# Kernel tuning notes

Measured on AMD Instinct MI355X. Metric: run time of the kernel, lower is better.

Reference implementation:

```python
import jax, jax.numpy as jnp
import numpy as np

G = 256       # number of graphs in batch
NPG = 400     # nodes per graph (hardcoded in module)
DEG = 32      # avg degree
FIN = 400     # input feature dim
H = 64        # hidden_channels
N = G * NPG
E = G * NPG * DEG


def _glorot(key, fan_in, fan_out):
    lim = float(np.sqrt(6.0 / (fan_in + fan_out)))
    return jax.random.uniform(key, (fan_in, fan_out), jnp.float32, -lim, lim)


def setup_inputs() -> dict:
    key = jax.random.key(0)
    ks = jax.random.split(key, 12)
    x = jax.random.normal(ks[0], (N, FIN), jnp.float32)
    # intra-graph random edges, then offset by graph id so edges never cross graphs
    src = jax.random.randint(ks[1], (G, NPG * DEG), 0, NPG)
    dst = jax.random.randint(ks[2], (G, NPG * DEG), 0, NPG)
    offs = (jnp.arange(G) * NPG)[:, None]
    edge_index = jnp.stack([(src + offs).reshape(-1), (dst + offs).reshape(-1)]).astype(jnp.int32)
    edge_weight = jax.random.uniform(ks[3], (E,), jnp.float32)
    return {
        "x": x,
        "edge_index": edge_index,
        "edge_weight": edge_weight,
        "W1": _glorot(ks[4], FIN, H), "b1": jnp.zeros((H,), jnp.float32),
        "W2": _glorot(ks[5], H, H),   "b2": jnp.zeros((H,), jnp.float32),
        "W3": _glorot(ks[6], H, H),   "b3": jnp.zeros((H,), jnp.float32),
        "Wc": _glorot(ks[7], NPG * H, H), "bc": jnp.zeros((H,), jnp.float32),
        "Wl": _glorot(ks[8], H, 2),   "bl": jnp.zeros((2,), jnp.float32),
    }


def _gcn_conv(x, W, b, row, col, norm, n):
    # PyG GCNConv: out[col] += norm * (x @ W)[row]; then + bias
    h = x @ W                                   # [n, out]
    msg = norm[:, None] * h[row]                # [E+n, out] gather + scale
    return jax.ops.segment_sum(msg, col, num_segments=n) + b


def reference(x, edge_index, edge_weight, W1, b1, W2, b2, W3, b3, Wc, bc, Wl, bl):
    n = x.shape[0]
    loop = jnp.arange(n, dtype=edge_index.dtype)
    row = jnp.concatenate([edge_index[0], loop])            # sources (with self-loops)
    col = jnp.concatenate([edge_index[1], loop])            # targets
    ew = jnp.concatenate([edge_weight, jnp.ones((n,), edge_weight.dtype)])
    # symmetric normalization: deg^{-1/2}[row] * w * deg^{-1/2}[col]
    deg = jax.ops.segment_sum(ew, col, num_segments=n)
    dinv = jnp.where(deg > 0, jax.lax.rsqrt(deg), 0.0)
    norm = dinv[row] * ew * dinv[col]

    h = jax.nn.relu(_gcn_conv(x, W1, b1, row, col, norm, n))
    h = jax.nn.relu(_gcn_conv(h, W2, b2, row, col, norm, n))
    h = _gcn_conv(h, W3, b3, row, col, norm, n)
    # per-graph flatten of 400 nodes -> lincomb (vectorized form of the Python loop)
    g = h.reshape(-1, NPG * H) @ Wc + bc        # [G, H]
    # dropout p=0.5 skipped (eval mode)
    return g @ Wl + bl                          # [G, 2]
```

## Files before the change

kernel.cpp:

```cpp
#include <hip/hip_runtime.h>
#include <hip/hip_bf16.h>
#include <stdint.h>

#define G 256
#define NPG 400
#define DEG 32
#define FIN 400
#define H 64
#define NN (G*NPG)
#define EE (G*NPG*DEG)
#define EPG (NPG*DEG)
#define CPG (EPG+NPG)
#define NTILE 25
#define ATS 420
#define HTS 72
#define MTSZ 25600

#define W1F_OFF 0
#define W1F_N   (13*4*64*8)
#define W2F_OFF (W1F_OFF + W1F_N)
#define W2F_N   (2*4*64*8)
#define W3F_OFF (W2F_OFF + W2F_N)
#define WCF_OFF (W3F_OFF + W2F_N)
#define WCF_N   (800*4*64*8)
#define WF_TOT  (WCF_OFF + WCF_N)

typedef __attribute__((ext_vector_type(8))) _Float16 h8;
typedef __attribute__((ext_vector_type(4))) float f32x4;

static __device__ __forceinline__ unsigned packh2(float a, float b) {
  unsigned short ua = __builtin_bit_cast(unsigned short, (_Float16)a);
  unsigned short ub = __builtin_bit_cast(unsigned short, (_Float16)b);
  return (unsigned)ua | ((unsigned)ub << 16);
}

static __device__ __forceinline__ h8 cvt8(float4 a, float4 b) {
  h8 r;
  r[0] = (_Float16)a.x; r[1] = (_Float16)a.y; r[2] = (_Float16)a.z; r[3] = (_Float16)a.w;
  r[4] = (_Float16)b.x; r[5] = (_Float16)b.y; r[6] = (_Float16)b.z; r[7] = (_Float16)b.w;
  return r;
}

__global__ __launch_bounds__(256) void kPack(
    const float* __restrict__ W1, const float* __restrict__ W2,
    const float* __restrict__ W3, const float* __restrict__ Wc,
    _Float16* __restrict__ wf, float* __restrict__ gbuf)
{
  int idx = blockIdx.x*256 + threadIdx.x;
  if (idx < G*H) gbuf[idx] = 0.f;
  if (idx >= WF_TOT) return;
  if (idx < W2F_OFF) {
    int i = idx;
    int j = i & 7, ln = (i >> 3) & 63, nt = (i >> 9) & 3, ks = i >> 11;
    int k = ks*32 + (ln >> 4)*8 + j, col = nt*16 + (ln & 15);
    wf[idx] = (k < FIN) ? (_Float16)W1[k*H + col] : (_Float16)0.f;
  } else if (idx < W3F_OFF) {
    int i = idx - W2F_OFF;
    int j = i & 7, ln = (i >> 3) & 63, nt = (i >> 9) & 3, ks = i >> 11;
    wf[idx] = (_Float16)W2[(ks*32 + (ln >> 4)*8 + j)*H + nt*16 + (ln & 15)];
  } else if (idx < WCF_OFF) {
    int i = idx - W3F_OFF;
    int j = i & 7, ln = (i >> 3) & 63, nt = (i >> 9) & 3, ks = i >> 11;
    wf[idx] = (_Float16)W3[(ks*32 + (ln >> 4)*8 + j)*H + nt*16 + (ln & 15)];
  } else {
    int i = idx - WCF_OFF;
    int j = i & 7, ln = (i >> 3) & 63, nt = (i >> 9) & 3, kt = i >> 11;
    int kp = kt*32 + (ln >> 4)*8 + j;
    int node = kp % 400, feat = kp / 400;
    int col = nt*16 + (ln & 15);
    wf[idx] = (_Float16)Wc[((size_t)node*64 + feat)*64 + col];
  }
}

__global__ __launch_bounds__(1024) void kNorm(
    const int* __restrict__ ei, const float* __restrict__ ew,
    uint2* __restrict__ ent, uint32_t* __restrict__ boff)
{
  __shared__ float deg[NPG];
  __shared__ float dv[NPG];
  __shared__ uint32_t bcnt[32], bpos[32];
  const int g = blockIdx.x, tid = threadIdx.x;
  const int ebase = g*EPG, nbase = g*NPG;
  const int* rowp = ei;
  const int* colp = ei + EE;
  if (tid < NTILE) bcnt[tid] = 0u;
  for (int v = tid; v < NPG; v += 1024) deg[v] = 1.0f;
  __syncthreads();
  for (int e = tid; e < EPG; e += 1024) {
    int c = colp[ebase+e] - nbase;
    atomicAdd(&deg[c], ew[ebase+e]);
    atomicAdd(&bcnt[c >> 4], 1u);
  }
  __syncthreads();
  for (int v = tid; v < NPG; v += 1024) dv[v] = rsqrtf(deg[v]);
  if (tid == 0) {
    uint32_t s = 0;
    #pragma unroll
    for (int t = 0; t < NTILE; ++t) {
      uint32_t c = bcnt[t] + 16u;
      bcnt[t] = s; bpos[t] = s; s += c;
    }
  }
  __syncthreads();
  if (tid < NTILE) boff[g*32 + tid] = bcnt[tid];
  if (tid == NTILE) boff[g*32 + NTILE] = (uint32_t)CPG;
  uint2* eb = ent + (size_t)g*CPG;
  for (int e = tid; e < EPG; e += 1024) {
    int src = rowp[ebase+e] - nbase;
    int dst = colp[ebase+e] - nbase;
    float nm = dv[src] * ew[ebase+e] * dv[dst];
    uint32_t p = atomicAdd(&bpos[dst >> 4], 1u);
    eb[p] = make_uint2(((unsigned)dst << 16) | (unsigned)src, __float_as_uint(nm));
  }
  for (int v = tid; v < NPG; v += 1024) {
    uint32_t p = atomicAdd(&bpos[v >> 4], 1u);
    eb[p] = make_uint2(((unsigned)v << 16) | (unsigned)v, __float_as_uint(dv[v]*dv[v]));
  }
}

__global__ __launch_bounds__(256, 4) void kM1(
    const float* __restrict__ x, const _Float16* __restrict__ wf,
    _Float16* __restrict__ mt1)
{
  __shared__ _Float16 sh[64*HTS];
  const int tid = threadIdx.x, lane = tid & 63, wave = tid >> 6;
  const int l15 = lane & 15, kgrp = lane >> 4;
  const int g = blockIdx.y, b = blockIdx.x;
  const int node_l = b*64 + wave*16 + l15;
  const int arow = (node_l < NPG) ? node_l : NPG-1;
  const float* xp = x + ((size_t)g*NPG + arow)*FIN;

  f32x4 acc[4] = {{0,0,0,0},{0,0,0,0},{0,0,0,0},{0,0,0,0}};
  for (int ks = 0; ks < 13; ++ks) {
    const int kb = ks*32 + kgrp*8;
    h8 af;
    if (kb + 8 <= FIN) {
      float4 a0 = *(const float4*)(xp + kb);
      float4 a1 = *(const float4*)(xp + kb + 4);
      af = cvt8(a0, a1);
    } else {
      h8 z;
      #pragma unroll
      for (int j = 0; j < 8; ++j) z[j] = (_Float16)0.f;
      af = z;
    }
    #pragma unroll
    for (int nt = 0; nt < 4; ++nt) {
      h8 bf = *(const h8*)&wf[W1F_OFF + (((size_t)ks*4 + nt)*64 + lane)*8];
      acc[nt] = __builtin_amdgcn_mfma_f32_16x16x32_f16(af, bf, acc[nt], 0, 0, 0);
    }
  }
  #pragma unroll
  for (int nt = 0; nt < 4; ++nt) {
    int feat = nt*16 + l15;
    #pragma unroll
    for (int r = 0; r < 4; ++r)
      sh[(wave*16 + kgrp*4 + r)*HTS + feat] = (_Float16)acc[nt][r];
  }
  __syncthreads();
  const unsigned short* shu = (const unsigned short*)sh;
  for (int i = tid; i < 64*16; i += 256) {
    int feat = i >> 4, seg = i & 15;
    int nl = seg*4, gn = b*64 + nl;
    if (gn < NPG) {
      uint2 u;
      u.x = (unsigned)shu[(nl+0)*HTS + feat] | ((unsigned)shu[(nl+1)*HTS + feat] << 16);
      u.y = (unsigned)shu[(nl+2)*HTS + feat] | ((unsigned)shu[(nl+3)*HTS + feat] << 16);
      *(uint2*)&mt1[(size_t)g*MTSZ + feat*400 + gn] = u;
    }
  }
}

template<int WMUL>
__global__ __launch_bounds__(256, 4) void kAgg(
    const _Float16* __restrict__ mtin, const _Float16* __restrict__ wfn,
    const float* __restrict__ bias,
    const uint2* __restrict__ ent, const uint32_t* __restrict__ boff,
    _Float16* __restrict__ out)
{
  extern __shared__ char smem[];
  float* sAT = (float*)smem;
  _Float16* sh = (_Float16*)(smem + 16*ATS*4);
  const int tid = threadIdx.x, lane = tid & 63;
  const int l15 = lane & 15, kgrp = lane >> 4;
  const int bid = blockIdx.x;
  const int g = bid & 255, t = bid >> 8;
  const int t0 = t*16;
  const int nt = tid >> 6;
  const uint2* eb = ent + (size_t)g*CPG;
  const uint32_t s0 = boff[g*32 + t], s1 = boff[g*32 + t + 1];

  h8 BF[13];
  const _Float16* mrow = mtin + (size_t)g*MTSZ + (nt*16 + l15)*400;
  #pragma unroll
  for (int ks = 0; ks < 13; ++ks)
    BF[ks] = *(const h8*)(mrow + ks*32 + kgrp*8);
  const float bv = bias[nt*16 + l15];
  h8 WF2[2];
  if (WMUL) {
    WF2[0] = *(const h8*)&wfn[((size_t)(0*4 + nt)*64 + lane)*8];
    WF2[1] = *(const h8*)&wfn[((size_t)(1*4 + nt)*64 + lane)*8];
  }
  const uint32_t e0 = s0 + tid;
  uint2 E0 = make_uint2(0,0), E1 = make_uint2(0,0), E2 = make_uint2(0,0);
  if (e0       < s1) E0 = eb[e0];
  if (e0 + 256 < s1) E1 = eb[e0 + 256];
  if (e0 + 512 < s1) E2 = eb[e0 + 512];

  { float4* p = (float4*)sAT;
    for (int i = tid; i < 16*ATS/4; i += 256) p[i] = make_float4(0,0,0,0); }
  __syncthreads();

  if (e0       < s1) atomicAdd(&sAT[((int)(E0.x >> 16) - t0)*ATS + (int)(E0.x & 0xffffu)], __uint_as_float(E0.y));
  if (e0 + 256 < s1) atomicAdd(&sAT[((int)(E1.x >> 16) - t0)*ATS + (int)(E1.x & 0xffffu)], __uint_as_float(E1.y));
  if (e0 + 512 < s1) atomicAdd(&sAT[((int)(E2.x >> 16) - t0)*ATS + (int)(E2.x & 0xffffu)], __uint_as_float(E2.y));
  for (uint32_t e = e0 + 768; e < s1; e += 256) {
    uint2 E = eb[e];
    atomicAdd(&sAT[((int)(E.x >> 16) - t0)*ATS + (int)(E.x & 0xffffu)], __uint_as_float(E.y));
  }
  __syncthreads();

  f32x4 acc = {0,0,0,0};
  const float* ap = &sAT[l15*ATS];
  #pragma unroll
  for (int ks = 0; ks < 13; ++ks) {
    int kb = ks*32 + kgrp*8;
    float4 a0 = *(const float4*)(ap + kb);
    float4 a1 = *(const float4*)(ap + kb + 4);
    acc = __builtin_amdgcn_mfma_f32_16x16x32_f16(cvt8(a0, a1), BF[ks], acc, 0, 0, 0);
  }

  const int node0 = t0 + kgrp*4;
  if (!WMUL) {
    uint2 u;
    u.x = packh2(acc[0] + bv, acc[1] + bv);
    u.y = packh2(acc[2] + bv, acc[3] + bv);
    *(uint2*)&out[(size_t)g*MTSZ + (nt*16 + l15)*400 + node0] = u;
  } else {
    #pragma unroll
    for (int r = 0; r < 4; ++r)
      sh[(kgrp*4 + r)*HTS + nt*16 + l15] = (_Float16)fmaxf(acc[r] + bv, 0.f);
    __syncthreads();
    f32x4 acc2 = {0,0,0,0};
    const _Float16* hp = &sh[l15*HTS];
    acc2 = __builtin_amdgcn_mfma_f32_16x16x32_f16(*(const h8*)(hp + kgrp*8),      WF2[0], acc2, 0, 0, 0);
    acc2 = __builtin_amdgcn_mfma_f32_16x16x32_f16(*(const h8*)(hp + 32 + kgrp*8), WF2[1], acc2, 0, 0, 0);
    uint2 u;
    u.x = packh2(acc2[0], acc2[1]);
    u.y = packh2(acc2[2], acc2[3]);
    *(uint2*)&out[(size_t)g*MTSZ + (nt*16 + l15)*400 + node0] = u;
  }
}

__global__ __launch_bounds__(256) void kRead(
    const _Float16* __restrict__ h3, const _Float16* __restrict__ wfc,
    float* __restrict__ gbuf)
{
  const int tid = threadIdx.x, lane = tid & 63, nt = tid >> 6;
  const int l15 = lane & 15, kgrp = lane >> 4;
  const int rt = blockIdx.x & 15, kc = blockIdx.x >> 4;
  f32x4 acc = {0,0,0,0};
  const _Float16* hp = h3 + (size_t)(rt*16 + l15)*MTSZ;
  for (int ks = 0; ks < 25; ++ks) {
    int kt = kc*25 + ks;
    h8 af = *(const h8*)(hp + kt*32 + kgrp*8);
    h8 bf = *(const h8*)(wfc + (((size_t)kt*4 + nt)*64 + lane)*8);
    acc = __builtin_amdgcn_mfma_f32_16x16x32_f16(af, bf, acc, 0, 0, 0);
  }
  #pragma unroll
  for (int r = 0; r < 4; ++r)
    atomicAdd(&gbuf[(size_t)(rt*16 + kgrp*4 + r)*H + nt*16 + l15], acc[r]);
}

__global__ __launch_bounds__(64) void k6_final(
    const float* __restrict__ gbuf, const float* __restrict__ bc,
    const float* __restrict__ Wl, const float* __restrict__ bl,
    float* __restrict__ out)
{
  int t = blockIdx.x*64 + threadIdx.x;
  int gr = t >> 1, c = t & 1;
  float acc = bl[c];
  for (int f = 0; f < H; ++f)
    acc += (gbuf[gr*H + f] + bc[f]) * Wl[f*2 + c];
  out[gr*2 + c] = acc;
}

extern "C" void kernel_launch(void* const* d_in, const int* in_sizes, int n_in,
                              void* d_out, int out_size, void* d_ws, size_t ws_size,
                              hipStream_t stream)
{
  const float* x  = (const float*)d_in[0];
  const int*   ei = (const int*)d_in[1];
  const float* ew = (const float*)d_in[2];
  const float* W1 = (const float*)d_in[3];
  const float* b1 = (const float*)d_in[4];
  const float* W2 = (const float*)d_in[5];
  const float* b2 = (const float*)d_in[6];
  const float* W3 = (const float*)d_in[7];
  const float* b3 = (const float*)d_in[8];
  const float* Wc = (const float*)d_in[9];
  const float* bc = (const float*)d_in[10];
  const float* Wl = (const float*)d_in[11];
  const float* bl = (const float*)d_in[12];
  float* out = (float*)d_out;
  (void)ws_size;

  char* ws = (char*)d_ws;
  size_t o = 0;
  uint2*     ent  = (uint2*)(ws + o);     o += (size_t)G*CPG*8;
  uint32_t*  boff = (uint32_t*)(ws + o);  o += (size_t)G*32*4;
  _Float16*  mtA  = (_Float16*)(ws + o);  o += (size_t)G*MTSZ*2 + 256;
  _Float16*  mtB  = (_Float16*)(ws + o);  o += (size_t)G*MTSZ*2 + 256;
  _Float16*  wf   = (_Float16*)(ws + o);  o += (size_t)WF_TOT*2;
  float*     gbuf = (float*)(ws + o);     o += (size_t)G*H*4;

  kPack<<<(WF_TOT+255)/256, 256, 0, stream>>>(W1, W2, W3, Wc, wf, gbuf);
  kNorm<<<G, 1024, 0, stream>>>(ei, ew, ent, boff);
  kM1<<<dim3(7, G), 256, 0, stream>>>(x, wf, mtA);
  const int aggLds = 16*ATS*4 + 16*HTS*2;
  kAgg<1><<<NTILE*G, 256, aggLds, stream>>>(mtA, wf + W2F_OFF, b1, ent, boff, mtB);
  kAgg<1><<<NTILE*G, 256, aggLds, stream>>>(mtB, wf + W3F_OFF, b2, ent, boff, mtA);
  kAgg<0><<<NTILE*G, 256, aggLds, stream>>>(mtA, wf, b3, ent, boff, mtB);
  kRead<<<512, 256, 0, stream>>>(mtB, wf + WCF_OFF, gbuf);
  k6_final<<<8, 64, 0, stream>>>(gbuf, bc, Wl, bl, out);
}
```

Before: 267.7 us.

## Store intermediate features in MFMA fragment layout and replace atomics with partial sums

Intermediate per-graph feature matrices are now written directly in the MFMA B-operand fragment order (padded to 416 nodes), so kM1 drops its LDS transpose and the aggregation kernels load each fragment as one contiguous vector. The Wc packing is remapped to match the new layout, with zero padding for the extra nodes. The readout writes per-chunk partial sums instead of global atomics, and the final kernel reduces them with wave shuffles, which also removes the gbuf zeroing. kM1 occupancy hint is raised. The cost is a larger workspace and a partial-sum buffer.

Result: no change. 265.6 us (-0.8%).

```diff
diff --git a/kernel.cpp b/kernel.cpp
--- a/kernel.cpp
+++ b/kernel.cpp
@@ -14,7 +14,7 @@
 #define NTILE 25
 #define ATS 420
 #define HTS 72
-#define MTSZ 25600
+#define MTF 26624
 
 #define W1F_OFF 0
 #define W1F_N   (13*4*64*8)
@@ -22,7 +22,7 @@
 #define W2F_N   (2*4*64*8)
 #define W3F_OFF (W2F_OFF + W2F_N)
 #define WCF_OFF (W3F_OFF + W2F_N)
-#define WCF_N   (800*4*64*8)
+#define WCF_N   (832*4*64*8)
 #define WF_TOT  (WCF_OFF + WCF_N)
 
 typedef __attribute__((ext_vector_type(8))) _Float16 h8;
@@ -44,10 +44,9 @@
 __global__ __launch_bounds__(256) void kPack(
     const float* __restrict__ W1, const float* __restrict__ W2,
     const float* __restrict__ W3, const float* __restrict__ Wc,
-    _Float16* __restrict__ wf, float* __restrict__ gbuf)
+    _Float16* __restrict__ wf)
 {
   int idx = blockIdx.x*256 + threadIdx.x;
-  if (idx < G*H) gbuf[idx] = 0.f;
   if (idx >= WF_TOT) return;
   if (idx < W2F_OFF) {
     int i = idx;
@@ -64,11 +63,16 @@
     wf[idx] = (_Float16)W3[(ks*32 + (ln >> 4)*8 + j)*H + nt*16 + (ln & 15)];
   } else {
     int i = idx - WCF_OFF;
-    int j = i & 7, ln = (i >> 3) & 63, nt = (i >> 9) & 3, kt = i >> 11;
+    int j = i & 7, ln = (i >> 3) & 63, ntc = (i >> 9) & 3, kt = i >> 11;
     int kp = kt*32 + (ln >> 4)*8 + j;
-    int node = kp % 400, feat = kp / 400;
-    int col = nt*16 + (ln & 15);
-    wf[idx] = (_Float16)Wc[((size_t)node*64 + feat)*64 + col];
+    int nt_m = kp / 6656, rem = kp % 6656;
+    int ks_m = rem >> 9, rem2 = rem & 511;
+    int lane_m = rem2 >> 3, j_m = rem2 & 7;
+    int node = ks_m*32 + (lane_m >> 4)*8 + j_m;
+    int feat = nt_m*16 + (lane_m & 15);
+    int col = ntc*16 + (ln & 15);
+    wf[idx] = (node < NPG) ? (_Float16)Wc[((size_t)node*64 + feat)*64 + col]
+                           : (_Float16)0.f;
   }
 }
 
@@ -118,11 +122,10 @@
   }
 }
 
-__global__ __launch_bounds__(256, 4) void kM1(
+__global__ __launch_bounds__(256, 8) void kM1(
     const float* __restrict__ x, const _Float16* __restrict__ wf,
     _Float16* __restrict__ mt1)
 {
-  __shared__ _Float16 sh[64*HTS];
   const int tid = threadIdx.x, lane = tid & 63, wave = tid >> 6;
   const int l15 = lane & 15, kgrp = lane >> 4;
   const int g = blockIdx.y, b = blockIdx.x;
@@ -150,23 +153,16 @@
       acc[nt] = __builtin_amdgcn_mfma_f32_16x16x32_f16(af, bf, acc[nt], 0, 0, 0);
     }
   }
-  #pragma unroll
-  for (int nt = 0; nt < 4; ++nt) {
-    int feat = nt*16 + l15;
+  const int nd0 = b*64 + wave*16 + kgrp*4;
+  if (nd0 < NPG) {
+    const int ksw = nd0 >> 5, lh = (nd0 >> 3) & 3, jb = nd0 & 7;
+    _Float16* mb = mt1 + (size_t)g*MTF;
     #pragma unroll
-    for (int r = 0; r < 4; ++r)
-      sh[(wave*16 + kgrp*4 + r)*HTS + feat] = (_Float16)acc[nt][r];
-  }
-  __syncthreads();
-  const unsigned short* shu = (const unsigned short*)sh;
-  for (int i = tid; i < 64*16; i += 256) {
-    int feat = i >> 4, seg = i & 15;
-    int nl = seg*4, gn = b*64 + nl;
-    if (gn < NPG) {
+    for (int nt = 0; nt < 4; ++nt) {
       uint2 u;
-      u.x = (unsigned)shu[(nl+0)*HTS + feat] | ((unsigned)shu[(nl+1)*HTS + feat] << 16);
-      u.y = (unsigned)shu[(nl+2)*HTS + feat] | ((unsigned)shu[(nl+3)*HTS + feat] << 16);
-      *(uint2*)&mt1[(size_t)g*MTSZ + feat*400 + gn] = u;
+      u.x = packh2(acc[nt][0], acc[nt][1]);
+      u.y = packh2(acc[nt][2], acc[nt][3]);
+      *(uint2*)&mb[(((size_t)nt*13 + ksw)*64 + lh*16 + l15)*8 + jb] = u;
     }
   }
 }
@@ -191,10 +187,10 @@
   const uint32_t s0 = boff[g*32 + t], s1 = boff[g*32 + t + 1];
 
   h8 BF[13];
-  const _Float16* mrow = mtin + (size_t)g*MTSZ + (nt*16 + l15)*400;
+  const _Float16* mrow = mtin + (size_t)g*MTF + (size_t)nt*13*512 + lane*8;
   #pragma unroll
   for (int ks = 0; ks < 13; ++ks)
-    BF[ks] = *(const h8*)(mrow + ks*32 + kgrp*8);
+    BF[ks] = *(const h8*)(mrow + ks*512);
   const float bv = bias[nt*16 + l15];
   h8 WF2[2];
   if (WMUL) {
@@ -230,12 +226,15 @@
     acc = __builtin_amdgcn_mfma_f32_16x16x32_f16(cvt8(a0, a1), BF[ks], acc, 0, 0, 0);
   }
 
-  const int node0 = t0 + kgrp*4;
+  const int nd0 = t0 + kgrp*4;
+  const int ksw = nd0 >> 5, lh = (nd0 >> 3) & 3, jb = nd0 & 7;
+  _Float16* ob = out + (size_t)g*MTF;
+
   if (!WMUL) {
     uint2 u;
     u.x = packh2(acc[0] + bv, acc[1] + bv);
     u.y = packh2(acc[2] + bv, acc[3] + bv);
-    *(uint2*)&out[(size_t)g*MTSZ + (nt*16 + l15)*400 + node0] = u;
+    *(uint2*)&ob[(((size_t)nt*13 + ksw)*64 + lh*16 + l15)*8 + jb] = u;
   } else {
     #pragma unroll
     for (int r = 0; r < 4; ++r)
@@ -248,41 +247,51 @@
     uint2 u;
     u.x = packh2(acc2[0], acc2[1]);
     u.y = packh2(acc2[2], acc2[3]);
-    *(uint2*)&out[(size_t)g*MTSZ + (nt*16 + l15)*400 + node0] = u;
+    *(uint2*)&ob[(((size_t)nt*13 + ksw)*64 + lh*16 + l15)*8 + jb] = u;
   }
 }
 
 __global__ __launch_bounds__(256) void kRead(
     const _Float16* __restrict__ h3, const _Float16* __restrict__ wfc,
-    float* __restrict__ gbuf)
+    float* __restrict__ gpart)
 {
   const int tid = threadIdx.x, lane = tid & 63, nt = tid >> 6;
   const int l15 = lane & 15, kgrp = lane >> 4;
   const int rt = blockIdx.x & 15, kc = blockIdx.x >> 4;
   f32x4 acc = {0,0,0,0};
-  const _Float16* hp = h3 + (size_t)(rt*16 + l15)*MTSZ;
-  for (int ks = 0; ks < 25; ++ks) {
-    int kt = kc*25 + ks;
+  const _Float16* hp = h3 + (size_t)(rt*16 + l15)*MTF;
+  for (int ks = 0; ks < 26; ++ks) {
+    int kt = kc*26 + ks;
     h8 af = *(const h8*)(hp + kt*32 + kgrp*8);
     h8 bf = *(const h8*)(wfc + (((size_t)kt*4 + nt)*64 + lane)*8);
     acc = __builtin_amdgcn_mfma_f32_16x16x32_f16(af, bf, acc, 0, 0, 0);
   }
   #pragma unroll
   for (int r = 0; r < 4; ++r)
-    atomicAdd(&gbuf[(size_t)(rt*16 + kgrp*4 + r)*H + nt*16 + l15], acc[r]);
+    gpart[((size_t)(kc*16 + rt)*16 + kgrp*4 + r)*64 + nt*16 + l15] = acc[r];
 }
 
 __global__ __launch_bounds__(64) void k6_final(
-    const float* __restrict__ gbuf, const float* __restrict__ bc,
+    const float* __restrict__ gpart, const float* __restrict__ bc,
     const float* __restrict__ Wl, const float* __restrict__ bl,
     float* __restrict__ out)
 {
-  int t = blockIdx.x*64 + threadIdx.x;
-  int gr = t >> 1, c = t & 1;
-  float acc = bl[c];
-  for (int f = 0; f < H; ++f)
-    acc += (gbuf[gr*H + f] + bc[f]) * Wl[f*2 + c];
-  out[gr*2 + c] = acc;
+  const int g = blockIdx.x, f = threadIdx.x;
+  float s = bc[f];
+  #pragma unroll 4
+  for (int kc = 0; kc < 32; ++kc)
+    s += gpart[((size_t)(kc*16 + (g >> 4))*16 + (g & 15))*64 + f];
+  float p0 = s * Wl[f*2 + 0];
+  float p1 = s * Wl[f*2 + 1];
+  #pragma unroll
+  for (int d = 1; d < 64; d <<= 1) {
+    p0 += __shfl_xor(p0, d);
+    p1 += __shfl_xor(p1, d);
+  }
+  if (f == 0) {
+    out[g*2 + 0] = p0 + bl[0];
+    out[g*2 + 1] = p1 + bl[1];
+  }
 }
 
 extern "C" void kernel_launch(void* const* d_in, const int* in_sizes, int n_in,
@@ -307,20 +316,20 @@
 
   char* ws = (char*)d_ws;
   size_t o = 0;
-  uint2*     ent  = (uint2*)(ws + o);     o += (size_t)G*CPG*8;
-  uint32_t*  boff = (uint32_t*)(ws + o);  o += (size_t)G*32*4;
-  _Float16*  mtA  = (_Float16*)(ws + o);  o += (size_t)G*MTSZ*2 + 256;
-  _Float16*  mtB  = (_Float16*)(ws + o);  o += (size_t)G*MTSZ*2 + 256;
-  _Float16*  wf   = (_Float16*)(ws + o);  o += (size_t)WF_TOT*2;
-  float*     gbuf = (float*)(ws + o);     o += (size_t)G*H*4;
-
-  kPack<<<(WF_TOT+255)/256, 256, 0, stream>>>(W1, W2, W3, Wc, wf, gbuf);
+  uint2*     ent   = (uint2*)(ws + o);     o += (size_t)G*CPG*8;
+  uint32_t*  boff  = (uint32_t*)(ws + o);  o += (size_t)G*32*4;
+  _Float16*  mtA   = (_Float16*)(ws + o);  o += (size_t)G*MTF*2 + 256;
+  _Float16*  mtB   = (_Float16*)(ws + o);  o += (size_t)G*MTF*2 + 256;
+  _Float16*  wf    = (_Float16*)(ws + o);  o += (size_t)WF_TOT*2;
+  float*     gpart = (float*)(ws + o);     o += (size_t)32*G*H*4;
+
+  kPack<<<WF_TOT/256, 256, 0, stream>>>(W1, W2, W3, Wc, wf);
   kNorm<<<G, 1024, 0, stream>>>(ei, ew, ent, boff);
   kM1<<<dim3(7, G), 256, 0, stream>>>(x, wf, mtA);
   const int aggLds = 16*ATS*4 + 16*HTS*2;
   kAgg<1><<<NTILE*G, 256, aggLds, stream>>>(mtA, wf + W2F_OFF, b1, ent, boff, mtB);
   kAgg<1><<<NTILE*G, 256, aggLds, stream>>>(mtB, wf + W3F_OFF, b2, ent, boff, mtA);
   kAgg<0><<<NTILE*G, 256, aggLds, stream>>>(mtA, wf, b3, ent, boff, mtB);
-  kRead<<<512, 256, 0, stream>>>(mtB, wf + WCF_OFF, gbuf);
-  k6_final<<<8, 64, 0, stream>>>(gbuf, bc, Wl, bl, out);
-}
+  kRead<<<512, 256, 0, stream>>>(mtB, wf + WCF_OFF, gpart);
+  k6_final<<<G, 64, 0, stream>>>(gpart, bc, Wl, bl, out);
+}
```
